# Optimization experiments

Hardware: AMD Instinct MI355X
Metric: run time of the kernel (lower is better)

Reference implementation:

```python
import jax, jax.numpy as jnp
import numpy as np

# Deterministic, fully-vectorized JAX version of the augmentation pipeline
# (labels=None branch). Randomness comes from a fixed PRNG key so the
# reference is reproducible. All per-sample PIL/CPU loops in the original
# are replaced by batched on-device ops: affine warp + hflip (geometric),
# brightness/contrast/saturation jitter (color), 3x3 gaussian blur,
# random erasing, GridMask, final clamp to [0,1].


def _affine_warp(x, key):
    """Batched inverse-mapped bilinear affine warp. x: [B,C,H,W]."""
    B, C, H, W = x.shape
    k1, k2, k3, k4 = jax.random.split(key, 4)
    deg = jnp.pi / 180.0
    ang = jax.random.uniform(k1, (B,), minval=-25.0, maxval=25.0) * deg
    shr = jax.random.uniform(k2, (B,), minval=-15.0, maxval=15.0) * deg
    scl = jax.random.uniform(k3, (B,), minval=0.85, maxval=1.15)
    trn = jax.random.uniform(k4, (B, 2), minval=-0.15, maxval=0.15)
    tx = trn[:, 0] * W
    ty = trn[:, 1] * H
    c, s = jnp.cos(ang), jnp.sin(ang)
    t = jnp.tan(shr)
    # inverse map (output pixel -> input pixel): shear^-1 @ rot^-1 / scale
    m00 = (c - t * (-s)) / scl
    m01 = (s - t * c) / scl
    m10 = (-s) / scl
    m11 = c / scl
    M = jnp.stack([jnp.stack([m00, m01], -1), jnp.stack([m10, m11], -1)], -2)  # [B,2,2]
    # centered pixel coordinate grid [2,H,W] (x, y)
    ys = jnp.arange(H, dtype=x.dtype) - (H - 1) / 2.0
    xs = jnp.arange(W, dtype=x.dtype) - (W - 1) / 2.0
    gy, gx = jnp.meshgrid(ys, xs, indexing='ij')
    grid = jnp.stack([gx, gy], 0)  # [2,H,W]
    src = jnp.einsum('bij,jhw->bihw', M, grid)  # [B,2,H,W]
    sx = src[:, 0] - tx[:, None, None] + (W - 1) / 2.0
    sy = src[:, 1] - ty[:, None, None] + (H - 1) / 2.0

    def sample_one(img, sx1, sy1):  # img [C,H,W]; sx1,sy1 [H,W]
        x0 = jnp.floor(sx1)
        y0 = jnp.floor(sy1)
        wx = sx1 - x0
        wy = sy1 - y0
        x0i = x0.astype(jnp.int32)
        y0i = y0.astype(jnp.int32)

        def g(yi, xi):
            valid = ((xi >= 0) & (xi < W) & (yi >= 0) & (yi < H)).astype(img.dtype)
            return img[:, jnp.clip(yi, 0, H - 1), jnp.clip(xi, 0, W - 1)] * valid

        return (g(y0i, x0i) * (1 - wx) * (1 - wy)
                + g(y0i, x0i + 1) * wx * (1 - wy)
                + g(y0i + 1, x0i) * (1 - wx) * wy
                + g(y0i + 1, x0i + 1) * wx * wy)

    return jax.vmap(sample_one)(x, sx, sy)


def _color_jitter(x, key):
    B = x.shape[0]
    kb, kc, ks = jax.random.split(key, 3)
    b = jax.random.uniform(kb, (B, 1, 1, 1), minval=0.7, maxval=1.3)
    c = jax.random.uniform(kc, (B, 1, 1, 1), minval=0.7, maxval=1.3)
    s = jax.random.uniform(ks, (B, 1, 1, 1), minval=0.8, maxval=1.2)
    x = x * b  # brightness
    mean = jnp.mean(x, axis=(1, 2, 3), keepdims=True)
    x = (x - mean) * c + mean  # contrast
    luma = jnp.array([0.299, 0.587, 0.114], x.dtype)
    gray = jnp.einsum('bchw,c->bhw', x, luma)[:, None]  # [B,1,H,W]
    x = gray + (x - gray) * s  # saturation
    return x


def _gaussian_blur3(x):
    C = x.shape[1]
    k1 = jnp.array([0.25, 0.5, 0.25], x.dtype)
    kern = jnp.outer(k1, k1)  # 3x3
    kern = jnp.tile(kern[None, None], (C, 1, 1, 1))  # [C,1,3,3] depthwise
    return jax.lax.conv_general_dilated(x, kern, (1, 1), 'SAME',
                                        feature_group_count=C,
                                        dimension_numbers=('NCHW', 'OIHW', 'NCHW'))


def _random_erasing(x, key):
    B, C, H, W = x.shape
    ka, kr, kt, kl, kv, kp = jax.random.split(key, 6)
    area = jax.random.uniform(ka, (B,), minval=0.02, maxval=0.1) * H * W
    ratio = jax.random.uniform(kr, (B,), minval=0.3, maxval=3.0)
    eh = jnp.clip(jnp.sqrt(area * ratio), 1, H)
    ew = jnp.clip(jnp.sqrt(area / ratio), 1, W)
    top = jax.random.uniform(kt, (B,)) * (H - eh)
    left = jax.random.uniform(kl, (B,)) * (W - ew)
    rows = jnp.arange(H, dtype=x.dtype)[None, :]
    cols = jnp.arange(W, dtype=x.dtype)[None, :]
    rmask = (rows >= top[:, None]) & (rows < (top + eh)[:, None])  # [B,H]
    cmask = (cols >= left[:, None]) & (cols < (left + ew)[:, None])  # [B,W]
    box = (rmask[:, None, :, None] & cmask[:, None, None, :])  # [B,1,H,W]
    fill = jax.random.uniform(kv, x.shape, dtype=x.dtype)  # value='random'
    apply = jax.random.bernoulli(kp, 0.3, (B, 1, 1, 1))
    return jnp.where(box & apply, fill, x)


def _grid_mask(x, key):
    B, C, H, W = x.shape
    kd, kp = jax.random.split(key)
    d = jnp.floor(jax.random.uniform(kd, (B,), minval=8.0, maxval=32.0))
    l = jnp.floor(d * 0.6)
    rows = jnp.arange(H, dtype=x.dtype)[None, :]
    cols = jnp.arange(W, dtype=x.dtype)[None, :]
    rh = jnp.mod(rows, d[:, None]) < l[:, None]  # [B,H]
    rw = jnp.mod(cols, d[:, None]) < l[:, None]  # [B,W]
    hole = rh[:, None, :, None] & rw[:, None, None, :]  # [B,1,H,W]
    apply = jax.random.bernoulli(kp, 0.3, (B, 1, 1, 1))
    return jnp.where(hole & apply, jnp.zeros_like(x), x)


def setup_inputs() -> dict:
    key = jax.random.key(0)
    x = jax.random.uniform(key, (2048, 3, 64, 64), dtype=jnp.float32)
    return {"x": x}


def reference(x) -> jnp.ndarray:
    B = x.shape[0]
    key = jax.random.key(42)
    kg, kf, kc, kb, ke, km = jax.random.split(key, 6)
    # geometric: affine warp + random horizontal flip (p=0.6)
    x = _affine_warp(x, kg)
    flip = jax.random.bernoulli(kf, 0.6, (B, 1, 1, 1))
    x = jnp.where(flip, x[..., ::-1], x)
    # color jitter
    x = _color_jitter(x, kc)
    # gaussian blur, applied per-sample with p=0.3
    blur = jax.random.bernoulli(kb, 0.3, (B, 1, 1, 1))
    x = jnp.where(blur, _gaussian_blur3(x), x)
    # random erasing
    x = _random_erasing(x, ke)
    # grid mask
    x = _grid_mask(x, km)
    return jnp.clip(x, 0.0, 1.0)
```

## Files before the change

kernel.cpp:

```cpp
#include <hip/hip_runtime.h>
#include <stdint.h>
#include <math.h>

#pragma clang fp contract(off)

struct KeyPair { uint32_t hi, lo; };
struct KTab { KeyPair k[17]; };

__host__ __device__ __forceinline__ uint32_t rotl32(uint32_t x, int r) {
  return (x << r) | (x >> (32 - r));
}

__host__ __device__ __forceinline__ void threefry2x32(uint32_t k0, uint32_t k1,
                                                      uint32_t x0, uint32_t x1,
                                                      uint32_t& o0, uint32_t& o1) {
  const uint32_t ks0 = k0, ks1 = k1, ks2 = k0 ^ k1 ^ 0x1BD11BDAu;
  x0 += ks0; x1 += ks1;
#define TF_R(r) { x0 += x1; x1 = rotl32(x1, (r)); x1 ^= x0; }
  TF_R(13) TF_R(15) TF_R(26) TF_R(6)
  x0 += ks1; x1 += ks2 + 1u;
  TF_R(17) TF_R(29) TF_R(16) TF_R(24)
  x0 += ks2; x1 += ks0 + 2u;
  TF_R(13) TF_R(15) TF_R(26) TF_R(6)
  x0 += ks0; x1 += ks1 + 3u;
  TF_R(17) TF_R(29) TF_R(16) TF_R(24)
  x0 += ks1; x1 += ks2 + 4u;
  TF_R(13) TF_R(15) TF_R(26) TF_R(6)
  x0 += ks2; x1 += ks0 + 5u;
#undef TF_R
  o0 = x0; o1 = x1;
}

__host__ __device__ __forceinline__ uint32_t jax_rbits32(KeyPair k, uint32_t i) {
  uint32_t a, b; threefry2x32(k.hi, k.lo, 0u, i, a, b);
  return a ^ b;
}

__host__ __device__ __forceinline__ KeyPair jax_split_child(KeyPair k, uint32_t j) {
  uint32_t a, b; threefry2x32(k.hi, k.lo, 0u, j, a, b);
  KeyPair r; r.hi = a; r.lo = b; return r;
}

__host__ __device__ __forceinline__ float bits_to_unit(uint32_t bits) {
  uint32_t fb = (bits >> 9) | 0x3F800000u;
  return __builtin_bit_cast(float, fb) - 1.0f;
}

__device__ __forceinline__ float map_u(float u, float mn, float mx) {
  return fmaxf(mn, u * (mx - mn) + mn);
}

struct SP {
  float m00, m01, m10, m11, txp, typ;
  float bb, cc, ssat;
  int flip, doblur, apply_e, apply_g;
};

#define RS  65
#define PLS 4360

__global__ __launch_bounds__(512, 4) void aug_kernel(const float* __restrict__ in,
                                                     float* __restrict__ out,
                                                     KTab KT, KeyPair kv, int B) {
  const int b = blockIdx.x;
  const int tid = threadIdx.x;
  __shared__ float simg[3 * PLS];
  __shared__ SP sp;
  __shared__ unsigned long long mgrid, merow, mecol;
  __shared__ float red[8];

  const float* __restrict__ inb = in + (size_t)b * 12288;

  float4 st[6];
#pragma unroll
  for (int it = 0; it < 6; ++it) st[it] = ((const float4*)inb)[tid + it * 512];

  if (tid < 64) {
    float myu = 0.f;
    if (tid < 17) {
      KeyPair k = KT.k[tid];
      uint32_t i = (tid == 3) ? 2u * (uint32_t)b
                 : (tid == 4) ? 2u * (uint32_t)b + 1u
                 : (uint32_t)b;
      myu = bits_to_unit(jax_rbits32(k, i));
    }
    float u[17];
#pragma unroll
    for (int j = 0; j < 17; ++j) u[j] = __shfl(myu, j);

    const float DEG = 0.017453292519943295f;
    const float ang = map_u(u[0], -25.f, 25.f) * DEG;
    const float shr = map_u(u[1], -15.f, 15.f) * DEG;
    const float scl = map_u(u[2], 0.85f, 1.15f);
    const float t_x = map_u(u[3], -0.15f, 0.15f) * 64.f;
    const float t_y = map_u(u[4], -0.15f, 0.15f) * 64.f;
    const float cA = cosf(ang), sA = sinf(ang), tS = tanf(shr);
    float area = map_u(u[10], 0.02f, 0.1f);
    area = area * 64.f;
    area = area * 64.f;
    const float ratio = map_u(u[11], 0.3f, 3.0f);
    const float eh = fminf(fmaxf(sqrtf(area * ratio), 1.f), 64.f);
    const float ew = fminf(fmaxf(sqrtf(area / ratio), 1.f), 64.f);
    const float topv = u[12] * (64.f - eh);
    const float leftv = u[13] * (64.f - ew);
    const float dG = floorf(map_u(u[15], 8.f, 32.f));
    const float lG = floorf(dG * 0.6f);

    const float rf = (float)tid;
    const unsigned long long g  = __ballot(fmodf(rf, dG) < lG);
    const unsigned long long er = __ballot((rf >= topv) & (rf < (topv + eh)));
    const unsigned long long ec = __ballot((rf >= leftv) & (rf < (leftv + ew)));
    if (tid == 0) {
      sp.m00 = (cA - tS * (-sA)) / scl;
      sp.m01 = (sA - tS * cA) / scl;
      sp.m10 = (-sA) / scl;
      sp.m11 = cA / scl;
      sp.txp = t_x; sp.typ = t_y;
      sp.flip = u[5] < 0.6f;
      sp.bb = map_u(u[6], 0.7f, 1.3f);
      sp.cc = map_u(u[7], 0.7f, 1.3f);
      sp.ssat = map_u(u[8], 0.8f, 1.2f);
      sp.doblur = u[9] < 0.3f;
      sp.apply_e = u[14] < 0.3f;
      sp.apply_g = u[16] < 0.3f;
      mgrid = g; merow = er; mecol = ec;
    }
  } else if (tid < 328) {
    const int z = tid - 64;
    int a;
    if (z < 65)       a = z;
    else if (z < 200) a = 4160 + z;
    else              a = (z - 199) * RS;
#pragma unroll
    for (int c = 0; c < 3; ++c) simg[c * PLS + a] = 0.f;
  }

#pragma unroll
  for (int it = 0; it < 6; ++it) {
    const int f = it * 2048 + tid * 4;
    const int c = f >> 12;
    const int r = (f >> 6) & 63;
    const int cc = f & 63;
    float* d = &simg[c * PLS + (r + 1) * RS + cc + 1];
    d[0] = st[it].x; d[1] = st[it].y; d[2] = st[it].z; d[3] = st[it].w;
  }
  __syncthreads();

  const float m00 = sp.m00, m01 = sp.m01, m10 = sp.m10, m11 = sp.m11;
  const float txp = sp.txp, typ = sp.typ;
  const float bb = sp.bb, cc = sp.cc, ssat = sp.ssat;
  const int flip = sp.flip, doblur = sp.doblur;
  const int apply_e = sp.apply_e, apply_g = sp.apply_g;
  const unsigned long long mg = mgrid, mer = merow, mec = mecol;

  float vv[3][8];
  float lsum = 0.f;
#pragma unroll
  for (int it = 0; it < 8; ++it) {
    const int p = tid + it * 512;
    const int h = p >> 6;
    const int w = p & 63;
    const int wsrc = flip ? (63 - w) : w;
    const float gx = (float)wsrc - 31.5f;
    const float gy = (float)h - 31.5f;
    float sx = (m00 * gx + m01 * gy) - txp + 31.5f;
    float sy = (m10 * gx + m11 * gy) - typ + 31.5f;
    sx = fminf(fmaxf(sx, -1.f), 64.f);
    sy = fminf(fmaxf(sy, -1.f), 64.f);
    const float fx0 = floorf(sx), fy0 = floorf(sy);
    const float wx = sx - fx0, wy = sy - fy0;
    const float omx = 1.f - wx, omy = 1.f - wy;
    const float w00 = omx * omy, w01 = wx * omy, w10 = omx * wy, w11 = wx * wy;
    const int a = ((int)fy0 + 1) * RS + (int)fx0 + 1;
#pragma unroll
    for (int c = 0; c < 3; ++c) {
      const float* t = &simg[c * PLS + a];
      const float v = t[0] * w00 + t[1] * w01 + t[RS] * w10 + t[RS + 1] * w11;
      vv[c][it] = v;
      lsum += v;
    }
  }
  {
    float wsum = lsum;
    for (int off = 32; off > 0; off >>= 1) wsum += __shfl_down(wsum, off);
    if ((tid & 63) == 0) red[tid >> 6] = wsum;
  }
  __syncthreads();

  const float mean = (bb * (red[0] + red[1] + red[2] + red[3] +
                            red[4] + red[5] + red[6] + red[7])) / 12288.f;
  const float Ac = ssat * cc * bb;
  const float Gc = (1.f - ssat) * cc * bb;
  const float mprime = mean * (1.f - cc);
  float* __restrict__ ob = out + (size_t)b * 12288;

  if (!doblur) {
#pragma unroll
    for (int it = 0; it < 8; ++it) {
      const int p = tid + it * 512;
      const int h = p >> 6, w = p & 63;
      const bool do_er = apply_e && ((mer >> h) & 1ull) && ((mec >> w) & 1ull);
      const bool do_gr = apply_g && ((mg >> h) & 1ull) && ((mg >> w) & 1ull);
      const float gray = 0.299f * vv[0][it] + 0.587f * vv[1][it] + 0.114f * vv[2][it];
#pragma unroll
      for (int c = 0; c < 3; ++c) {
        float v = Ac * vv[c][it] + Gc * gray + mprime;
        if (do_er) {
          const uint32_t idx = ((uint32_t)(b * 3 + c) << 12) | (uint32_t)p;
          v = bits_to_unit(jax_rbits32(kv, idx));
        }
        if (do_gr) v = 0.f;
        ob[c * 4096 + p] = fminf(fmaxf(v, 0.f), 1.f);
      }
    }
  } else {
#pragma unroll
    for (int it = 0; it < 8; ++it) {
      const int p = tid + it * 512;
      const int a = ((p >> 6) + 1) * RS + (p & 63) + 1;
#pragma unroll
      for (int c = 0; c < 3; ++c) simg[c * PLS + a] = vv[c][it];
    }
    __syncthreads();
#pragma unroll 1
    for (int it = 0; it < 2; ++it) {
      const int qq = tid + it * 512;
      const int h = qq >> 4;
      const int w0 = (qq & 15) * 4;
      float px[3][4];
#pragma unroll
      for (int c = 0; c < 3; ++c) {
        float win[3][6];
#pragma unroll
        for (int r = 0; r < 3; ++r) {
          const float* row = &simg[c * PLS + (h + r) * RS + w0 + 1];
#pragma unroll
          for (int k = 0; k < 6; ++k) win[r][k] = row[k - 1];
        }
#pragma unroll
        for (int j = 0; j < 4; ++j) {
          const float h0 = 0.25f * win[0][j] + 0.5f * win[0][j + 1] + 0.25f * win[0][j + 2];
          const float h1 = 0.25f * win[1][j] + 0.5f * win[1][j + 1] + 0.25f * win[1][j + 2];
          const float h2 = 0.25f * win[2][j] + 0.5f * win[2][j + 1] + 0.25f * win[2][j + 2];
          px[c][j] = 0.25f * h0 + 0.5f * h1 + 0.25f * h2;
        }
      }
      const float rowe = (h == 0 || h == 63) ? 0.75f : 1.f;
      const bool erow_b = apply_e && ((mer >> h) & 1ull);
      const bool grow_b = apply_g && ((mg >> h) & 1ull);
      float o[3][4];
#pragma unroll
      for (int j = 0; j < 4; ++j) {
        const int w = w0 + j;
        const float gray = 0.299f * px[0][j] + 0.587f * px[1][j] + 0.114f * px[2][j];
        const float cole = (w == 0 || w == 63) ? 0.75f : 1.f;
        const float moff = mprime * (rowe * cole);
        const bool do_er = erow_b && ((mec >> w) & 1ull);
        const bool do_gr = grow_b && ((mg >> w) & 1ull);
#pragma unroll
        for (int c = 0; c < 3; ++c) {
          float v = Ac * px[c][j] + Gc * gray + moff;
          if (do_er) {
            const uint32_t idx = ((uint32_t)(b * 3 + c) << 12) | (uint32_t)(h << 6) | (uint32_t)w;
            v = bits_to_unit(jax_rbits32(kv, idx));
          }
          if (do_gr) v = 0.f;
          o[c][j] = fminf(fmaxf(v, 0.f), 1.f);
        }
      }
#pragma unroll
      for (int c = 0; c < 3; ++c) {
        float4 stv; stv.x = o[c][0]; stv.y = o[c][1]; stv.z = o[c][2]; stv.w = o[c][3];
        *(float4*)&ob[c * 4096 + h * 64 + w0] = stv;
      }
    }
  }
}

extern "C" void kernel_launch(void* const* d_in, const int* in_sizes, int n_in,
                              void* d_out, int out_size, void* d_ws, size_t ws_size,
                              hipStream_t stream) {
  (void)n_in; (void)out_size; (void)d_ws; (void)ws_size;
  const float* x = (const float*)d_in[0];
  float* out = (float*)d_out;
  const int B = in_sizes[0] / (3 * 64 * 64);
  if (B <= 0) return;

  KeyPair root; root.hi = 0u; root.lo = 42u;
  KeyPair kg = jax_split_child(root, 0);
  KeyPair kf = jax_split_child(root, 1);
  KeyPair kc = jax_split_child(root, 2);
  KeyPair kb = jax_split_child(root, 3);
  KeyPair ke = jax_split_child(root, 4);
  KeyPair km = jax_split_child(root, 5);

  KTab KT;
  KT.k[0]  = jax_split_child(kg, 0);
  KT.k[1]  = jax_split_child(kg, 1);
  KT.k[2]  = jax_split_child(kg, 2);
  KT.k[3]  = jax_split_child(kg, 3);
  KT.k[4]  = KT.k[3];
  KT.k[5]  = kf;
  KT.k[6]  = jax_split_child(kc, 0);
  KT.k[7]  = jax_split_child(kc, 1);
  KT.k[8]  = jax_split_child(kc, 2);
  KT.k[9]  = kb;
  KT.k[10] = jax_split_child(ke, 0);
  KT.k[11] = jax_split_child(ke, 1);
  KT.k[12] = jax_split_child(ke, 2);
  KT.k[13] = jax_split_child(ke, 3);
  KT.k[14] = jax_split_child(ke, 5);
  KT.k[15] = jax_split_child(km, 0);
  KT.k[16] = jax_split_child(km, 1);
  KeyPair kv = jax_split_child(ke, 4);

  aug_kernel<<<dim3(B), dim3(512), 0, stream>>>(x, out, KT, kv, B);
}
```

Measured before the change: 186.6 us.

## Drop shared-memory image staging; gather bilinear taps directly from global memory

Removes the 52KB padded shared-memory image tile. Bilinear taps are now gathered straight from global input through the cache, and per-sample parameters are computed redundantly in every wavefront instead of broadcast through shared memory. The blur path stages intermediate values in the global output buffer rather than in LDS. This frees LDS so more blocks can be resident and removes one barrier, at the cost of scattered global or L2 gathers and extra global traffic on the blur path.

```diff
diff --git a/kernel.cpp b/kernel.cpp
--- a/kernel.cpp
+++ b/kernel.cpp
@@ -50,108 +50,62 @@
   return fmaxf(mn, u * (mx - mn) + mn);
 }
 
-struct SP {
-  float m00, m01, m10, m11, txp, typ;
-  float bb, cc, ssat;
-  int flip, doblur, apply_e, apply_g;
-};
-
-#define RS  65
-#define PLS 4360
-
 __global__ __launch_bounds__(512, 4) void aug_kernel(const float* __restrict__ in,
                                                      float* __restrict__ out,
                                                      KTab KT, KeyPair kv, int B) {
   const int b = blockIdx.x;
   const int tid = threadIdx.x;
-  __shared__ float simg[3 * PLS];
-  __shared__ SP sp;
-  __shared__ unsigned long long mgrid, merow, mecol;
+  const int lane = tid & 63;
   __shared__ float red[8];
 
   const float* __restrict__ inb = in + (size_t)b * 12288;
-
-  float4 st[6];
-#pragma unroll
-  for (int it = 0; it < 6; ++it) st[it] = ((const float4*)inb)[tid + it * 512];
-
-  if (tid < 64) {
-    float myu = 0.f;
-    if (tid < 17) {
-      KeyPair k = KT.k[tid];
-      uint32_t i = (tid == 3) ? 2u * (uint32_t)b
-                 : (tid == 4) ? 2u * (uint32_t)b + 1u
-                 : (uint32_t)b;
-      myu = bits_to_unit(jax_rbits32(k, i));
-    }
-    float u[17];
-#pragma unroll
-    for (int j = 0; j < 17; ++j) u[j] = __shfl(myu, j);
-
-    const float DEG = 0.017453292519943295f;
-    const float ang = map_u(u[0], -25.f, 25.f) * DEG;
-    const float shr = map_u(u[1], -15.f, 15.f) * DEG;
-    const float scl = map_u(u[2], 0.85f, 1.15f);
-    const float t_x = map_u(u[3], -0.15f, 0.15f) * 64.f;
-    const float t_y = map_u(u[4], -0.15f, 0.15f) * 64.f;
-    const float cA = cosf(ang), sA = sinf(ang), tS = tanf(shr);
-    float area = map_u(u[10], 0.02f, 0.1f);
-    area = area * 64.f;
-    area = area * 64.f;
-    const float ratio = map_u(u[11], 0.3f, 3.0f);
-    const float eh = fminf(fmaxf(sqrtf(area * ratio), 1.f), 64.f);
-    const float ew = fminf(fmaxf(sqrtf(area / ratio), 1.f), 64.f);
-    const float topv = u[12] * (64.f - eh);
-    const float leftv = u[13] * (64.f - ew);
-    const float dG = floorf(map_u(u[15], 8.f, 32.f));
-    const float lG = floorf(dG * 0.6f);
-
-    const float rf = (float)tid;
-    const unsigned long long g  = __ballot(fmodf(rf, dG) < lG);
-    const unsigned long long er = __ballot((rf >= topv) & (rf < (topv + eh)));
-    const unsigned long long ec = __ballot((rf >= leftv) & (rf < (leftv + ew)));
-    if (tid == 0) {
-      sp.m00 = (cA - tS * (-sA)) / scl;
-      sp.m01 = (sA - tS * cA) / scl;
-      sp.m10 = (-sA) / scl;
-      sp.m11 = cA / scl;
-      sp.txp = t_x; sp.typ = t_y;
-      sp.flip = u[5] < 0.6f;
-      sp.bb = map_u(u[6], 0.7f, 1.3f);
-      sp.cc = map_u(u[7], 0.7f, 1.3f);
-      sp.ssat = map_u(u[8], 0.8f, 1.2f);
-      sp.doblur = u[9] < 0.3f;
-      sp.apply_e = u[14] < 0.3f;
-      sp.apply_g = u[16] < 0.3f;
-      mgrid = g; merow = er; mecol = ec;
-    }
-  } else if (tid < 328) {
-    const int z = tid - 64;
-    int a;
-    if (z < 65)       a = z;
-    else if (z < 200) a = 4160 + z;
-    else              a = (z - 199) * RS;
-#pragma unroll
-    for (int c = 0; c < 3; ++c) simg[c * PLS + a] = 0.f;
-  }
-
-#pragma unroll
-  for (int it = 0; it < 6; ++it) {
-    const int f = it * 2048 + tid * 4;
-    const int c = f >> 12;
-    const int r = (f >> 6) & 63;
-    const int cc = f & 63;
-    float* d = &simg[c * PLS + (r + 1) * RS + cc + 1];
-    d[0] = st[it].x; d[1] = st[it].y; d[2] = st[it].z; d[3] = st[it].w;
-  }
-  __syncthreads();
-
-  const float m00 = sp.m00, m01 = sp.m01, m10 = sp.m10, m11 = sp.m11;
-  const float txp = sp.txp, typ = sp.typ;
-  const float bb = sp.bb, cc = sp.cc, ssat = sp.ssat;
-  const int flip = sp.flip, doblur = sp.doblur;
-  const int apply_e = sp.apply_e, apply_g = sp.apply_g;
-  const unsigned long long mg = mgrid, mer = merow, mec = mecol;
+  float* __restrict__ ob = out + (size_t)b * 12288;
+
+  float myu = 0.f;
+  if (lane < 17) {
+    KeyPair k = KT.k[lane];
+    uint32_t i = (lane == 3) ? 2u * (uint32_t)b
+               : (lane == 4) ? 2u * (uint32_t)b + 1u
+               : (uint32_t)b;
+    myu = bits_to_unit(jax_rbits32(k, i));
+  }
+  float u[17];
+#pragma unroll
+  for (int j = 0; j < 17; ++j) u[j] = __shfl(myu, j);
+
+  const float DEG = 0.017453292519943295f;
+  const float ang = map_u(u[0], -25.f, 25.f) * DEG;
+  const float shr = map_u(u[1], -15.f, 15.f) * DEG;
+  const float scl = map_u(u[2], 0.85f, 1.15f);
+  const float txp = map_u(u[3], -0.15f, 0.15f) * 64.f;
+  const float typ = map_u(u[4], -0.15f, 0.15f) * 64.f;
+  const float cA = cosf(ang), sA = sinf(ang), tS = tanf(shr);
+  const float m00 = (cA - tS * (-sA)) / scl;
+  const float m01 = (sA - tS * cA) / scl;
+  const float m10 = (-sA) / scl;
+  const float m11 = cA / scl;
+  const int flip = u[5] < 0.6f;
+  const float bb = map_u(u[6], 0.7f, 1.3f);
+  const float cc = map_u(u[7], 0.7f, 1.3f);
+  const float ssat = map_u(u[8], 0.8f, 1.2f);
+  const int doblur = u[9] < 0.3f;
+  float area = map_u(u[10], 0.02f, 0.1f);
+  area = area * 64.f;
+  area = area * 64.f;
+  const float ratio = map_u(u[11], 0.3f, 3.0f);
+  const float eh = fminf(fmaxf(sqrtf(area * ratio), 1.f), 64.f);
+  const float ew = fminf(fmaxf(sqrtf(area / ratio), 1.f), 64.f);
+  const float topv = u[12] * (64.f - eh);
+  const float leftv = u[13] * (64.f - ew);
+  const int apply_e = u[14] < 0.3f;
+  const float dG = floorf(map_u(u[15], 8.f, 32.f));
+  const float lG = floorf(dG * 0.6f);
+  const int apply_g = u[16] < 0.3f;
+
+  const float rf = (float)lane;
+  const unsigned long long mg  = __ballot(fmodf(rf, dG) < lG);
+  const unsigned long long mer = __ballot((rf >= topv) & (rf < (topv + eh)));
+  const unsigned long long mec = __ballot((rf >= leftv) & (rf < (leftv + ew)));
 
   float vv[3][8];
   float lsum = 0.f;
@@ -163,19 +117,30 @@
     const int wsrc = flip ? (63 - w) : w;
     const float gx = (float)wsrc - 31.5f;
     const float gy = (float)h - 31.5f;
-    float sx = (m00 * gx + m01 * gy) - txp + 31.5f;
-    float sy = (m10 * gx + m11 * gy) - typ + 31.5f;
-    sx = fminf(fmaxf(sx, -1.f), 64.f);
-    sy = fminf(fmaxf(sy, -1.f), 64.f);
+    const float sx = (m00 * gx + m01 * gy) - txp + 31.5f;
+    const float sy = (m10 * gx + m11 * gy) - typ + 31.5f;
     const float fx0 = floorf(sx), fy0 = floorf(sy);
     const float wx = sx - fx0, wy = sy - fy0;
+    const int x0 = (int)fx0, y0 = (int)fy0;
+    const int x1 = x0 + 1, y1 = y0 + 1;
+    const bool vx0 = (x0 >= 0) & (x0 < 64);
+    const bool vx1 = (x1 >= 0) & (x1 < 64);
+    const bool vy0 = (y0 >= 0) & (y0 < 64);
+    const bool vy1 = (y1 >= 0) & (y1 < 64);
+    const int x0c = min(max(x0, 0), 63), x1c = min(max(x1, 0), 63);
+    const int y0c = min(max(y0, 0), 63), y1c = min(max(y1, 0), 63);
+    const int a00 = y0c * 64 + x0c, a01 = y0c * 64 + x1c;
+    const int a10 = y1c * 64 + x0c, a11 = y1c * 64 + x1c;
     const float omx = 1.f - wx, omy = 1.f - wy;
     const float w00 = omx * omy, w01 = wx * omy, w10 = omx * wy, w11 = wx * wy;
-    const int a = ((int)fy0 + 1) * RS + (int)fx0 + 1;
 #pragma unroll
     for (int c = 0; c < 3; ++c) {
-      const float* t = &simg[c * PLS + a];
-      const float v = t[0] * w00 + t[1] * w01 + t[RS] * w10 + t[RS + 1] * w11;
+      const float* bp = inb + c * 4096;
+      const float t00 = (vy0 & vx0) ? bp[a00] : 0.f;
+      const float t01 = (vy0 & vx1) ? bp[a01] : 0.f;
+      const float t10 = (vy1 & vx0) ? bp[a10] : 0.f;
+      const float t11 = (vy1 & vx1) ? bp[a11] : 0.f;
+      const float v = t00 * w00 + t01 * w01 + t10 * w10 + t11 * w11;
       vv[c][it] = v;
       lsum += v;
     }
@@ -183,7 +148,7 @@
   {
     float wsum = lsum;
     for (int off = 32; off > 0; off >>= 1) wsum += __shfl_down(wsum, off);
-    if ((tid & 63) == 0) red[tid >> 6] = wsum;
+    if (lane == 0) red[tid >> 6] = wsum;
   }
   __syncthreads();
 
@@ -192,7 +157,6 @@
   const float Ac = ssat * cc * bb;
   const float Gc = (1.f - ssat) * cc * bb;
   const float mprime = mean * (1.f - cc);
-  float* __restrict__ ob = out + (size_t)b * 12288;
 
   if (!doblur) {
 #pragma unroll
@@ -217,12 +181,13 @@
 #pragma unroll
     for (int it = 0; it < 8; ++it) {
       const int p = tid + it * 512;
-      const int a = ((p >> 6) + 1) * RS + (p & 63) + 1;
-#pragma unroll
-      for (int c = 0; c < 3; ++c) simg[c * PLS + a] = vv[c][it];
+#pragma unroll
+      for (int c = 0; c < 3; ++c) ob[c * 4096 + p] = vv[c][it];
     }
     __syncthreads();
-#pragma unroll 1
+
+    float o[2][3][4];
+#pragma unroll
     for (int it = 0; it < 2; ++it) {
       const int qq = tid + it * 512;
       const int h = qq >> 4;
@@ -233,9 +198,16 @@
         float win[3][6];
 #pragma unroll
         for (int r = 0; r < 3; ++r) {
-          const float* row = &simg[c * PLS + (h + r) * RS + w0 + 1];
-#pragma unroll
-          for (int k = 0; k < 6; ++k) win[r][k] = row[k - 1];
+          const int hh = h - 1 + r;
+          if (hh >= 0 && hh <= 63) {
+            const float* row = ob + c * 4096 + hh * 64;
+            const float4 c4 = *(const float4*)&row[w0];
+            win[r][1] = c4.x; win[r][2] = c4.y; win[r][3] = c4.z; win[r][4] = c4.w;
+            win[r][0] = (w0 > 0)  ? row[w0 - 1] : 0.f;
+            win[r][5] = (w0 < 60) ? row[w0 + 4] : 0.f;
+          } else {
+            win[r][0] = win[r][1] = win[r][2] = win[r][3] = win[r][4] = win[r][5] = 0.f;
+          }
         }
 #pragma unroll
         for (int j = 0; j < 4; ++j) {
@@ -248,7 +220,6 @@
       const float rowe = (h == 0 || h == 63) ? 0.75f : 1.f;
       const bool erow_b = apply_e && ((mer >> h) & 1ull);
       const bool grow_b = apply_g && ((mg >> h) & 1ull);
-      float o[3][4];
 #pragma unroll
       for (int j = 0; j < 4; ++j) {
         const int w = w0 + j;
@@ -265,12 +236,20 @@
             v = bits_to_unit(jax_rbits32(kv, idx));
           }
           if (do_gr) v = 0.f;
-          o[c][j] = fminf(fmaxf(v, 0.f), 1.f);
-        }
-      }
+          o[it][c][j] = fminf(fmaxf(v, 0.f), 1.f);
+        }
+      }
+    }
+    __syncthreads();
+#pragma unroll
+    for (int it = 0; it < 2; ++it) {
+      const int qq = tid + it * 512;
+      const int h = qq >> 4;
+      const int w0 = (qq & 15) * 4;
 #pragma unroll
       for (int c = 0; c < 3; ++c) {
-        float4 stv; stv.x = o[c][0]; stv.y = o[c][1]; stv.z = o[c][2]; stv.w = o[c][3];
+        float4 stv;
+        stv.x = o[it][c][0]; stv.y = o[it][c][1]; stv.z = o[it][c][2]; stv.w = o[it][c][3];
         *(float4*)&ob[c * 4096 + h * 64 + w0] = stv;
       }
     }
```

Measured after the change: 309.1 us. 65.7% more time.
